# Kernel optimization log

Hardware: AMD Instinct MI355X
Metric: run time of the kernel (lower is better)

Reference implementation:

```python
import jax, jax.numpy as jnp
import numpy as np

IN_DIM = 512
OUT_DIM = 512
B = 2
N = 50000


def setup_inputs() -> dict:
    key = jax.random.key(0)
    k_z, k_s, k_m = jax.random.split(key, 3)
    z = jax.random.normal(k_z, (B, N, IN_DIM), dtype=jnp.float32)
    s = jax.random.normal(k_s, (B, OUT_DIM), dtype=jnp.float32)
    # torch_geometric uniform(in_dim, mat): U(-1/sqrt(in_dim), 1/sqrt(in_dim))
    bound = 1.0 / np.sqrt(IN_DIM)
    mat = jax.random.uniform(k_m, (IN_DIM, OUT_DIM), dtype=jnp.float32,
                             minval=-bound, maxval=bound)
    return {"z": z, "s": s, "mat": mat}


def reference(z, s, mat):
    # (z @ mat * s[:, None, :]).sum(dim=2).sigmoid()
    # z: [B, N, in_dim], mat: [in_dim, out_dim], s: [B, out_dim] -> [B, N]
    scores = jnp.einsum('bnd,de,be->bn', z, mat, s)
    return jax.nn.sigmoid(scores)
```

## Files before the change

### kernel.cpp

```cpp
#include <hip/hip_runtime.h>
#include <math.h>

#define IN_DIM  512
#define OUT_DIM 512
#define BATCH   2
#define NPTS    50000
#define TOTAL   (BATCH * NPTS)
#define RPW     16
#define NWAVES  (TOTAL / RPW)

typedef float f4 __attribute__((ext_vector_type(4)));

__device__ __forceinline__ f4 ntload(const f4* p) {
    return __builtin_nontemporal_load(p);
}

__device__ __forceinline__ float dot8(f4 a0, f4 a1, f4 b0, f4 b1) {
    return a0[0]*b0[0] + a0[1]*b0[1] + a0[2]*b0[2] + a0[3]*b0[3]
         + a1[0]*b1[0] + a1[1]*b1[1] + a1[2]*b1[2] + a1[3]*b1[3];
}

__device__ __forceinline__ float wred(float x) {
    #pragma unroll
    for (int off = 32; off; off >>= 1) x += __shfl_xor(x, off);
    return x;
}

__device__ __forceinline__ float sigmoidf(float x) {
    return 1.0f / (1.0f + __expf(-x));
}

__global__ __launch_bounds__(256) void dgi_compute_v(
    const float* __restrict__ mat, const float* __restrict__ s,
    float* __restrict__ v)
{
    const int lane = threadIdx.x & 63;
    const int W    = (int)((blockIdx.x * blockDim.x + threadIdx.x) >> 6);
    const int b    = W >> 9;
    const int d    = W & 511;

    const f4* mrow = reinterpret_cast<const f4*>(mat + (size_t)d * OUT_DIM);
    const f4* srow = reinterpret_cast<const f4*>(s   + (size_t)b * OUT_DIM);
    const f4 m0 = mrow[lane], m1 = mrow[lane + 64];
    const f4 s0 = srow[lane], s1 = srow[lane + 64];

    float acc = wred(dot8(m0, m1, s0, s1));
    if (lane == 0) v[b * IN_DIM + d] = acc;
}

__global__ __launch_bounds__(256, 8) void dgi_score(
    const float* __restrict__ z, const float* __restrict__ v,
    float* __restrict__ out)
{
    const int lane = threadIdx.x & 63;
    const int wid  = (int)((blockIdx.x * blockDim.x + threadIdx.x) >> 6);
    if (wid >= NWAVES) return;

    const long r0 = (long)wid * RPW;
    const int  b  = (r0 >= NPTS);

    const f4* vr = reinterpret_cast<const f4*>(v + (size_t)b * IN_DIM);
    const f4 v0 = vr[lane], v1 = vr[lane + 64];

    const f4* zp = reinterpret_cast<const f4*>(z + r0 * IN_DIM);

    f4 a0 = ntload(zp + lane),        a1 = ntload(zp + lane + 64);
    f4 c0 = ntload(zp + 128 + lane),  c1 = ntload(zp + 128 + lane + 64);

    #pragma unroll
    for (int i = 0; i < RPW; i += 2) {
        f4 n0, n1, n2, n3;
        if (i + 2 < RPW) {
            const f4* znA = zp + (i + 2) * 128;
            const f4* znB = zp + (i + 3) * 128;
            n0 = ntload(znA + lane);  n1 = ntload(znA + lane + 64);
            n2 = ntload(znB + lane);  n3 = ntload(znB + lane + 64);
        }
        float accA = wred(dot8(a0, a1, v0, v1));
        float accB = wred(dot8(c0, c1, v0, v1));
        if (lane == 0) {
            out[r0 + i]     = sigmoidf(accA);
            out[r0 + i + 1] = sigmoidf(accB);
        }
        a0 = n0; a1 = n1; c0 = n2; c1 = n3;
    }
}

extern "C" void kernel_launch(void* const* d_in, const int* in_sizes, int n_in,
                              void* d_out, int out_size, void* d_ws, size_t ws_size,
                              hipStream_t stream) {
    const float* z   = (const float*)d_in[0];
    const float* s   = (const float*)d_in[1];
    const float* mat = (const float*)d_in[2];
    float* out = (float*)d_out;
    float* v   = (float*)d_ws;

    dgi_compute_v<<<BATCH * 128, 256, 0, stream>>>(mat, s, v);

    const int blocks = (NWAVES + 3) / 4;
    dgi_score<<<blocks, 256, 0, stream>>>(z, v, out);
}
```

Before: 41.42 us.

## Load four rows per batch without software prefetch and vectorize output stores

Replaces the two-row software-pipelined prefetch loop with batches that issue loads for four rows at once, reduce all four, then write them from lanes 0-3 in one store. It also drops the minimum-blocks-per-CU hint from launch bounds. The aim is to keep more memory requests in flight per wave and cut serialized single-lane stores. The risk is that without cross-iteration prefetch the loads and reductions no longer overlap within a wave, and that register use may rise and lower occupancy.

New measurement: 41.28 us. No clear change (-0.4%).

```diff
diff --git a/kernel.cpp b/kernel.cpp
--- a/kernel.cpp
+++ b/kernel.cpp
@@ -48,7 +48,7 @@
     if (lane == 0) v[b * IN_DIM + d] = acc;
 }
 
-__global__ __launch_bounds__(256, 8) void dgi_score(
+__global__ __launch_bounds__(256) void dgi_score(
     const float* __restrict__ z, const float* __restrict__ v,
     float* __restrict__ out)
 {
@@ -64,25 +64,24 @@
 
     const f4* zp = reinterpret_cast<const f4*>(z + r0 * IN_DIM);
 
-    f4 a0 = ntload(zp + lane),        a1 = ntload(zp + lane + 64);
-    f4 c0 = ntload(zp + 128 + lane),  c1 = ntload(zp + 128 + lane + 64);
+    #pragma unroll
+    for (int i = 0; i < RPW; i += 4) {
+        const f4* zA = zp + (i + 0) * 128;
+        const f4* zB = zp + (i + 1) * 128;
+        const f4* zC = zp + (i + 2) * 128;
+        const f4* zD = zp + (i + 3) * 128;
+        const f4 a0 = ntload(zA + lane), a1 = ntload(zA + lane + 64);
+        const f4 b0 = ntload(zB + lane), b1 = ntload(zB + lane + 64);
+        const f4 c0 = ntload(zC + lane), c1 = ntload(zC + lane + 64);
+        const f4 d0 = ntload(zD + lane), d1 = ntload(zD + lane + 64);
 
-    #pragma unroll
-    for (int i = 0; i < RPW; i += 2) {
-        f4 n0, n1, n2, n3;
-        if (i + 2 < RPW) {
-            const f4* znA = zp + (i + 2) * 128;
-            const f4* znB = zp + (i + 3) * 128;
-            n0 = ntload(znA + lane);  n1 = ntload(znA + lane + 64);
-            n2 = ntload(znB + lane);  n3 = ntload(znB + lane + 64);
-        }
-        float accA = wred(dot8(a0, a1, v0, v1));
-        float accB = wred(dot8(c0, c1, v0, v1));
-        if (lane == 0) {
-            out[r0 + i]     = sigmoidf(accA);
-            out[r0 + i + 1] = sigmoidf(accB);
-        }
-        a0 = n0; a1 = n1; c0 = n2; c1 = n3;
+        const float rA = wred(dot8(a0, a1, v0, v1));
+        const float rB = wred(dot8(b0, b1, v0, v1));
+        const float rC = wred(dot8(c0, c1, v0, v1));
+        const float rD = wred(dot8(d0, d1, v0, v1));
+
+        float r = (lane == 0) ? rA : (lane == 1) ? rB : (lane == 2) ? rC : rD;
+        if (lane < 4) out[r0 + i + lane] = sigmoidf(r);
     }
 }
 
```
